# Optimization experiments

Measured on AMD Instinct MI355X. Metric: run time of the kernel, lower is better.

The kernel has to match this reference:

```python
import jax, jax.numpy as jnp
import numpy as np

TEMP = 0.07


def setup_inputs() -> dict:
    key = jax.random.key(0)
    kq, kk = jax.random.split(key)
    B, D = 8192, 128
    q = jax.random.normal(kq, (B, D), dtype=jnp.float32)
    k = jax.random.normal(kk, (B, D), dtype=jnp.float32)
    return {"q": q, "k": k}


def reference(q, k):
    # features = cat([q, k], dim=0); F.normalize(dim=1)
    B = q.shape[0]
    N = 2 * B
    f = jnp.concatenate([q, k], axis=0)
    f = f / jnp.maximum(jnp.linalg.norm(f, axis=1, keepdims=True), 1e-12)
    sim = f @ f.T  # [N, N]

    i = jnp.arange(N)
    p = (i + B) % N                      # index of the positive pair of row i
    pos = sim[i, p][:, None]             # [N, 1]

    # negatives: all columns except the diagonal (i) and the positive (p),
    # in original column order (matches boolean-mask ordering in torch).
    a = jnp.minimum(i, p)[:, None]       # [N, 1]
    b = jnp.maximum(i, p)[:, None]
    j = jnp.arange(N - 2)[None, :]       # [1, N-2]
    c = j + (j >= a)                     # skip first excluded column
    c = c + (c >= b)                     # skip second excluded column
    neg = jnp.take_along_axis(sim, c, axis=1)  # [N, N-2]

    logits = jnp.concatenate([pos, neg], axis=1) / TEMP  # [N, N-1]
    labels = jnp.zeros((N,), dtype=jnp.int32)
    return logits, labels
```

## Files before the change

### kernel.cpp

```cpp
#include <hip/hip_runtime.h>
#include <hip/hip_bf16.h>
#include <stdint.h>

#define B_ROWS 8192
#define N_TOT  16384
#define D_DIM  128
#define SCALE_SQRT_INVT 3.7796447300922722f

typedef __bf16 bf16x8 __attribute__((ext_vector_type(8)));
typedef float  f32x4  __attribute__((ext_vector_type(4)));

__global__ void simclr_norm_kernel(const float* __restrict__ q,
                                   const float* __restrict__ k,
                                   unsigned int* __restrict__ fb) {
    const int lane = threadIdx.x & 63;
    const int row  = blockIdx.x * 4 + (threadIdx.x >> 6);
    const float* src = (row < B_ROWS) ? (q + (size_t)row * D_DIM)
                                      : (k + (size_t)(row - B_ROWS) * D_DIM);
    float2 v = ((const float2*)src)[lane];
    float s = v.x * v.x + v.y * v.y;
#pragma unroll
    for (int off = 32; off > 0; off >>= 1) s += __shfl_xor(s, off);
    float rn = SCALE_SQRT_INVT / fmaxf(sqrtf(s), 1e-12f);
    union { __bf16 h[2]; unsigned int u; } pk;
    pk.h[0] = (__bf16)(v.x * rn);
    pk.h[1] = (__bf16)(v.y * rn);
    fb[(size_t)row * 64 + lane] = pk.u;
}

__global__ __launch_bounds__(256, 2) void simclr_gemm_kernel(
        const unsigned short* __restrict__ fb, float* __restrict__ out) {
    __shared__ char lds[65536];

    const int brow = blockIdx.x >> 7;
    const int bcol = blockIdx.x & 127;
    const int tid  = threadIdx.x;
    const int lane = tid & 63;
    const int w    = tid >> 6;

    {
        const int chunk = lane & 15;
        const int rsub  = lane >> 4;
#pragma unroll
        for (int i = 0; i < 8; ++i) {
            const int r = w * 32 + i * 4 + rsub;
            const int src_chunk = chunk ^ (r & 7);
            const char* gA = (const char*)(fb + ((size_t)(brow * 128 + r) * D_DIM + src_chunk * 8));
            const char* gB = (const char*)(fb + ((size_t)(bcol * 128 + r) * D_DIM + src_chunk * 8));
            char* lA = lds + (w * 32 + i * 4) * 256;
            char* lB = lds + 32768 + (w * 32 + i * 4) * 256;
            __builtin_amdgcn_global_load_lds((const __attribute__((address_space(1))) void*)gA,
                                             (__attribute__((address_space(3))) void*)lA, 16, 0, 0);
            __builtin_amdgcn_global_load_lds((const __attribute__((address_space(1))) void*)gB,
                                             (__attribute__((address_space(3))) void*)lB, 16, 0, 0);
        }
    }
    __syncthreads();

    const int wr = w >> 1, wc = w & 1;
    const int rl = lane & 15;
    const int kg = lane >> 4;

    f32x4 acc[4][4];
#pragma unroll
    for (int m = 0; m < 4; ++m)
#pragma unroll
        for (int n = 0; n < 4; ++n) acc[m][n] = (f32x4){0.f, 0.f, 0.f, 0.f};

#pragma unroll
    for (int ks = 0; ks < 4; ++ks) {
        bf16x8 afr[4], bfr[4];
        const int kb = ks * 64 + kg * 16;
#pragma unroll
        for (int m = 0; m < 4; ++m) {
            const int r = wr * 64 + m * 16 + rl;
            afr[m] = *(const bf16x8*)(lds + r * 256 + (kb ^ ((r & 7) << 4)));
        }
#pragma unroll
        for (int n = 0; n < 4; ++n) {
            const int r = wc * 64 + n * 16 + rl;
            bfr[n] = *(const bf16x8*)(lds + 32768 + r * 256 + (kb ^ ((r & 7) << 4)));
        }
#pragma unroll
        for (int m = 0; m < 4; ++m)
#pragma unroll
            for (int n = 0; n < 4; ++n)
                acc[m][n] = __builtin_amdgcn_mfma_f32_16x16x32_bf16(bfr[n], afr[m], acc[m][n], 0, 0, 0);
    }

    const int i_base = brow * 128 + wr * 64 + rl;
    const int c_base = bcol * 128 + wc * 64 + (kg << 2);
#pragma unroll
    for (int m = 0; m < 4; ++m) {
        const int i = i_base + m * 16;
        const int p = i ^ B_ROWS;
        const int a = i & (B_ROWS - 1);
        const int b = a | B_ROWS;
        float* orow = out + (size_t)i * (N_TOT - 1);
#pragma unroll
        for (int n = 0; n < 4; ++n) {
            const int c = c_base + n * 16;
            f32x4 v = acc[m][n];
            if (__builtin_expect((unsigned)(a - c) < 4u || (unsigned)(b - c) < 4u, 0)) {
#pragma unroll
                for (int e = 0; e < 4; ++e) {
                    const int cc = c + e;
                    const float val = v[e];
                    if (cc == i) continue;
                    if (cc == p) { orow[0] = val; continue; }
                    orow[cc + 1 - (cc > a) - (cc > b)] = val;
                }
            } else {
                const int s = 1 - (c > a) - (c > b);
                __builtin_memcpy(orow + c + s, &v, sizeof(v));
            }
        }
    }
}

__global__ void simclr_zero_labels(float* __restrict__ out) {
    out[(size_t)N_TOT * (N_TOT - 1) + blockIdx.x * 256 + threadIdx.x] = 0.0f;
}

extern "C" void kernel_launch(void* const* d_in, const int* in_sizes, int n_in,
                              void* d_out, int out_size, void* d_ws, size_t ws_size,
                              hipStream_t stream) {
    const float* q = (const float*)d_in[0];
    const float* k = (const float*)d_in[1];
    float* out = (float*)d_out;
    unsigned int* fb = (unsigned int*)d_ws;

    simclr_norm_kernel<<<N_TOT / 4, 256, 0, stream>>>(q, k, fb);
    simclr_zero_labels<<<N_TOT / 256, 256, 0, stream>>>(out);
    simclr_gemm_kernel<<<128 * 128, 256, 0, stream>>>((const unsigned short*)d_ws, out);
}
```

Baseline: 366.0 us.

## Load GEMM fragments directly from global memory, drop LDS staging, remap blocks

The GEMM kernel no longer stages A and B tiles through 64KB of LDS with a barrier. Each wave now reads its bf16 fragments straight from global memory, relying on L2 reuse. Occupancy is raised to 4 blocks per SM, and block indices are remapped so that consecutive blocks are spread across XCD-style groups. This removes the LDS round trip and the barrier, but wave pairs now read duplicate data from global or L2 instead of sharing it.

```diff
diff --git a/kernel.cpp b/kernel.cpp
--- a/kernel.cpp
+++ b/kernel.cpp
@@ -28,38 +28,23 @@
     fb[(size_t)row * 64 + lane] = pk.u;
 }
 
-__global__ __launch_bounds__(256, 2) void simclr_gemm_kernel(
+__global__ __launch_bounds__(256, 4) void simclr_gemm_kernel(
         const unsigned short* __restrict__ fb, float* __restrict__ out) {
-    __shared__ char lds[65536];
+    const int bid = blockIdx.x;
+    const int o   = (bid & 7) * 2048 + (bid >> 3);
+    const int brow = o >> 7;
+    const int bcol = o & 127;
 
-    const int brow = blockIdx.x >> 7;
-    const int bcol = blockIdx.x & 127;
     const int tid  = threadIdx.x;
     const int lane = tid & 63;
     const int w    = tid >> 6;
-
-    {
-        const int chunk = lane & 15;
-        const int rsub  = lane >> 4;
-#pragma unroll
-        for (int i = 0; i < 8; ++i) {
-            const int r = w * 32 + i * 4 + rsub;
-            const int src_chunk = chunk ^ (r & 7);
-            const char* gA = (const char*)(fb + ((size_t)(brow * 128 + r) * D_DIM + src_chunk * 8));
-            const char* gB = (const char*)(fb + ((size_t)(bcol * 128 + r) * D_DIM + src_chunk * 8));
-            char* lA = lds + (w * 32 + i * 4) * 256;
-            char* lB = lds + 32768 + (w * 32 + i * 4) * 256;
-            __builtin_amdgcn_global_load_lds((const __attribute__((address_space(1))) void*)gA,
-                                             (__attribute__((address_space(3))) void*)lA, 16, 0, 0);
-            __builtin_amdgcn_global_load_lds((const __attribute__((address_space(1))) void*)gB,
-                                             (__attribute__((address_space(3))) void*)lB, 16, 0, 0);
-        }
-    }
-    __syncthreads();
-
     const int wr = w >> 1, wc = w & 1;
     const int rl = lane & 15;
     const int kg = lane >> 4;
+
+    const char* fbb   = (const char*)fb;
+    const char* abase = fbb + ((size_t)(brow * 128 + wr * 64 + rl) * 256 + kg * 16);
+    const char* bbase = fbb + ((size_t)(bcol * 128 + wc * 64 + rl) * 256 + kg * 16);
 
     f32x4 acc[4][4];
 #pragma unroll
@@ -70,17 +55,12 @@
 #pragma unroll
     for (int ks = 0; ks < 4; ++ks) {
         bf16x8 afr[4], bfr[4];
-        const int kb = ks * 64 + kg * 16;
 #pragma unroll
-        for (int m = 0; m < 4; ++m) {
-            const int r = wr * 64 + m * 16 + rl;
-            afr[m] = *(const bf16x8*)(lds + r * 256 + (kb ^ ((r & 7) << 4)));
-        }
+        for (int m = 0; m < 4; ++m)
+            afr[m] = *(const bf16x8*)(abase + (size_t)m * 16 * 256 + ks * 64);
 #pragma unroll
-        for (int n = 0; n < 4; ++n) {
-            const int r = wc * 64 + n * 16 + rl;
-            bfr[n] = *(const bf16x8*)(lds + 32768 + r * 256 + (kb ^ ((r & 7) << 4)));
-        }
+        for (int n = 0; n < 4; ++n)
+            bfr[n] = *(const bf16x8*)(bbase + (size_t)n * 16 * 256 + ks * 64);
 #pragma unroll
         for (int m = 0; m < 4; ++m)
 #pragma unroll
```

After: 456.5 us. 1.25x slower.
